# Kernel optimization log

Hardware: AMD Instinct MI355X
Metric: run time of the kernel (lower is better)

## Reference

```python
import jax, jax.numpy as jnp
import numpy as np

N_NODES = 50000
K_CHEB = 3


def _norm_weights(edge_index, num_nodes):
    # PyG ChebConv with normalization='sym', lambda_max=2.0:
    # L_hat = (2/lambda_max) * (I - D^-1/2 A D^-1/2) - I = -D^-1/2 A D^-1/2
    src, dst = edge_index[0], edge_index[1]
    ones = jnp.ones(src.shape[0], dtype=jnp.float32)
    deg = jax.ops.segment_sum(ones, src, num_segments=num_nodes)
    dis = jnp.where(deg > 0, jax.lax.rsqrt(jnp.maximum(deg, 1.0)), 0.0)
    w = dis[src] * dis[dst]  # [E]
    return src, dst, w


def _cheb_conv(x, src, dst, w, W, b, num_nodes):
    # W: [K, in, out], b: [out]
    def lap(v):  # L_hat @ v = -(D^-1/2 A D^-1/2) v via gather + segment-sum
        return -jax.ops.segment_sum(w[:, None] * v[src], dst, num_segments=num_nodes)
    Tx0 = x
    out = Tx0 @ W[0]
    Tx1 = lap(x)
    out = out + Tx1 @ W[1]
    for k in range(2, W.shape[0]):
        Tx2 = 2.0 * lap(Tx1) - Tx0
        out = out + Tx2 @ W[k]
        Tx0, Tx1 = Tx1, Tx2
    return out + b


def setup_inputs() -> dict:
    key = jax.random.key(0)
    ks = jax.random.split(key, 9)
    N, E, F_IN, F_HID, F_OUT = N_NODES, 800000, 128, 64, 16
    x = jax.random.normal(ks[0], (N, F_IN), dtype=jnp.float32)
    edge_index = jax.random.randint(ks[1], (2, E), 0, N, dtype=jnp.int64)
    def glorot(k, kk, fi, fo):
        s = (6.0 / (fi + fo)) ** 0.5
        return jax.random.uniform(k, (kk, fi, fo), jnp.float32, -s, s)
    W1 = glorot(ks[2], K_CHEB, F_IN, F_HID)
    b1 = jnp.zeros((F_HID,), jnp.float32)
    Wm = glorot(ks[3], K_CHEB, F_HID, F_HID)
    bm = jnp.zeros((F_HID,), jnp.float32)
    W2 = glorot(ks[4], K_CHEB, F_HID, F_OUT)
    b2 = jnp.zeros((F_OUT,), jnp.float32)
    return {"x": x, "edge_index": edge_index, "W1": W1, "b1": b1,
            "Wm": Wm, "bm": bm, "W2": W2, "b2": b2}


def reference(x, edge_index, W1, b1, Wm, bm, W2, b2):
    src, dst, w = _norm_weights(edge_index, N_NODES)
    h = jax.nn.relu(_cheb_conv(x, src, dst, w, W1, b1, N_NODES))
    # dropout is identity in eval mode (training=False)
    h = jax.nn.relu(_cheb_conv(h, src, dst, w, Wm, bm, N_NODES))
    out = _cheb_conv(h, src, dst, w, W2, b2, N_NODES)
    return out
```

## Files before the change

### kernel.cpp

```cpp
#include <hip/hip_runtime.h>
#include <hip/hip_fp16.h>

constexpr int NNODES = 50000;
constexpr int NS  = 64;
constexpr int NR  = 4;
constexpr int RSZ = 12500;

typedef _Float16 half8_t __attribute__((ext_vector_type(8)));
typedef _Float16 half4_t __attribute__((ext_vector_type(4)));
typedef float    f32x4_t __attribute__((ext_vector_type(4)));

template<int CH> struct hvec_sel;
template<> struct hvec_sel<4> { using T = half4_t; };
template<> struct hvec_sel<8> { using T = half8_t; };


__global__ void __launch_bounds__(256) hist_kernel(const int* __restrict__ ei, int E, int ES,
                                                   int* __restrict__ part_src,
                                                   int* __restrict__ part_dst) {
  __shared__ int sh[RSZ];
  for (int i = threadIdx.x; i < RSZ; i += 256) sh[i] = 0;
  __syncthreads();
  const int s = blockIdx.x, r = blockIdx.y, z = blockIdx.z;
  const int lo = r * RSZ;
  const int* __restrict__ idxarr = ei + (z ? E : 0);
  const int e0 = s * ES, e1 = min(e0 + ES, E);
  for (int e = e0 + (int)threadIdx.x; e < e1; e += 256) {
    unsigned u = (unsigned)(idxarr[e] - lo);
    if (u < (unsigned)RSZ) atomicAdd(&sh[u], 1);
  }
  __syncthreads();
  int* __restrict__ part = z ? part_dst : part_src;
  const int base = (s * NR + r) * RSZ;
  for (int i = threadIdx.x; i < RSZ; i += 256) part[base + i] = sh[i];
}

__global__ void __launch_bounds__(256) reduce_kernel(const int* __restrict__ part_src,
                                                     int* __restrict__ part_dst,
                                                     float* __restrict__ dis,
                                                     int* __restrict__ cnt_dst, int N) {
  int n = blockIdx.x * 256 + threadIdx.x;
  if (n >= N) return;
  int r = n / RSZ, i = n - r * RSZ;
  int ssum = 0;
  #pragma unroll 4
  for (int s = 0; s < NS; ++s) ssum += part_src[(size_t)(s * NR + r) * RSZ + i];
  dis[n] = (ssum > 0) ? rsqrtf((float)ssum) : 0.0f;
  int off = 0;
  for (int s = 0; s < NS; ++s) {
    size_t idx = (size_t)(s * NR + r) * RSZ + i;
    int c = part_dst[idx];
    part_dst[idx] = off;
    off += c;
  }
  cnt_dst[n] = off;
}

__global__ void __launch_bounds__(256) scan1_kernel(const int* __restrict__ cnt,
                                                    int* __restrict__ exc,
                                                    int* __restrict__ bsum, int N) {
  __shared__ int sh[256];
  int tid = threadIdx.x;
  int i = blockIdx.x * 256 + tid;
  int v = (i < N) ? cnt[i] : 0;
  int acc = v;
  sh[tid] = acc; __syncthreads();
  #pragma unroll
  for (int off = 1; off < 256; off <<= 1) {
    int t = (tid >= off) ? sh[tid - off] : 0;
    __syncthreads();
    acc += t;
    sh[tid] = acc;
    __syncthreads();
  }
  if (i < N) exc[i] = acc - v;
  if (tid == 255) bsum[blockIdx.x] = acc;
}

__global__ void __launch_bounds__(256) scan2_kernel(int* __restrict__ bsum, int NB) {
  __shared__ int sh[256];
  int tid = threadIdx.x;
  int v = (tid < NB) ? bsum[tid] : 0;
  int acc = v;
  sh[tid] = acc; __syncthreads();
  #pragma unroll
  for (int off = 1; off < 256; off <<= 1) {
    int t = (tid >= off) ? sh[tid - off] : 0;
    __syncthreads();
    acc += t;
    sh[tid] = acc;
    __syncthreads();
  }
  if (tid < NB) bsum[tid] = acc - v;
}

__global__ void __launch_bounds__(256) scan3_kernel(int* __restrict__ exc,
                                                    const int* __restrict__ bsum, int N) {
  int i = blockIdx.x * 256 + threadIdx.x;
  if (i < N) exc[i] += bsum[blockIdx.x];
}

__global__ void __launch_bounds__(256) fill_kernel(const int* __restrict__ ei, int E, int ES,
                                                   const int* __restrict__ startv,
                                                   const int* __restrict__ pd_off,
                                                   const float* __restrict__ dis,
                                                   int2* __restrict__ ew) {
  __shared__ int cur[RSZ];
  for (int i = threadIdx.x; i < RSZ; i += 256) cur[i] = 0;
  __syncthreads();
  const int s = blockIdx.x, r = blockIdx.y;
  const int lo = r * RSZ;
  const int base = (s * NR + r) * RSZ;
  const int e0 = s * ES, e1 = min(e0 + ES, E);
  for (int e = e0 + (int)threadIdx.x; e < e1; e += 256) {
    int sv = ei[e], d = ei[E + e];
    unsigned u = (unsigned)(d - lo);
    if (u < (unsigned)RSZ) {
      int rank = atomicAdd(&cur[u], 1);
      int pos = startv[d] + pd_off[base + u] + rank;
      float w = -dis[sv] * dis[d];
      ew[pos] = make_int2(sv, __float_as_int(w));
    }
  }
}

template<int FIN, int FOUT>
__global__ void __launch_bounds__(256) pack_kernel(const float* __restrict__ W,
                                                   _Float16* __restrict__ Bp) {
  constexpr int NT = 3 * FOUT / 16;
  constexpr int KT = FIN / 32;
  const int total = KT * NT * 512;
  for (int i = blockIdx.x * 256 + threadIdx.x; i < total; i += gridDim.x * 256) {
    int j = i & 7;
    int lane = (i >> 3) & 63;
    int tile = i >> 9;
    int nt = tile % NT, kt = tile / NT;
    int k = kt * 32 + (lane >> 4) * 8 + j;
    int n = nt * 16 + (lane & 15);
    int cheb = n / FOUT, c = n - cheb * FOUT;
    Bp[i] = (_Float16)W[((size_t)cheb * FIN + k) * FOUT + c];
  }
}

template<int FIN, int FOUT, typename IN_T>
__global__ void __launch_bounds__(256) gemm_mfma_kernel(const IN_T* __restrict__ X,
    const _Float16* __restrict__ Bp, const float* __restrict__ b,
    _Float16* __restrict__ A, _Float16* __restrict__ U, _Float16* __restrict__ V, int N) {
  constexpr int NT = 3 * FOUT / 16;
  constexpr int C3 = NT / 3;
  constexpr int KT = FIN / 32;
  constexpr int LDR = FIN + 8;
  __shared__ _Float16 xs[64 * LDR];

  const int tid = threadIdx.x;
  const int row0 = blockIdx.x * 64;

  for (int i = tid * 4; i < 64 * FIN; i += 1024) {
    int r = i / FIN, k = i - r * FIN;
    int row = row0 + r;
    short4 hv = make_short4(0, 0, 0, 0);
    if (row < N) {
      if constexpr (sizeof(IN_T) == 4) {
        float4 v = *(const float4*)((const float*)X + (size_t)row * FIN + k);
        _Float16 h0 = (_Float16)v.x, h1 = (_Float16)v.y, h2 = (_Float16)v.z, h3 = (_Float16)v.w;
        hv = make_short4(*(short*)&h0, *(short*)&h1, *(short*)&h2, *(short*)&h3);
      } else {
        hv = *(const short4*)((const _Float16*)X + (size_t)row * FIN + k);
      }
    }
    *(short4*)(&xs[r * LDR + k]) = hv;
  }
  __syncthreads();

  const int wave = tid >> 6, lane = tid & 63;
  const int m = lane & 15, quad = lane >> 4;

  f32x4_t acc[NT];
  #pragma unroll
  for (int nt = 0; nt < NT; ++nt) acc[nt] = (f32x4_t){0.f, 0.f, 0.f, 0.f};

  #pragma unroll
  for (int kt = 0; kt < KT; ++kt) {
    half8_t a = *(const half8_t*)(&xs[(wave * 16 + m) * LDR + kt * 32 + quad * 8]);
    const half8_t* bp = (const half8_t*)Bp + (size_t)(kt * NT) * 64 + lane;
    #pragma unroll
    for (int nt = 0; nt < NT; ++nt) {
      half8_t bf = bp[(size_t)nt * 64];
      acc[nt] = __builtin_amdgcn_mfma_f32_16x16x32_f16(a, bf, acc[nt], 0, 0, 0);
    }
  }

  const int row_b = row0 + wave * 16 + quad * 4;
  #pragma unroll
  for (int nt = 0; nt < C3; ++nt) {
    int c = nt * 16 + m;
    float bb = b[c];
    #pragma unroll
    for (int r = 0; r < 4; ++r) {
      int row = row_b + r;
      if (row < N) {
        size_t o = (size_t)row * FOUT + c;
        A[o] = (_Float16)(acc[nt][r] - acc[nt + 2 * C3][r] + bb);
        U[o] = (_Float16)acc[nt + C3][r];
        V[o] = (_Float16)acc[nt + 2 * C3][r];
      }
    }
  }
}


template<int F, int CH>
__global__ void __launch_bounds__(256) lapA_kernel(const void* __restrict__ Vp,
    const void* __restrict__ Up, void* __restrict__ Yp,
    const int* __restrict__ start, const int* __restrict__ cnt,
    const int2* __restrict__ ew, int N) {
  using HT = typename hvec_sel<CH>::T;
  constexpr int H = F / CH;
  const HT* __restrict__ Vv = (const HT*)Vp;
  int t = blockIdx.x * 256 + threadIdx.x;
  int n = t / H;
  if (n >= N) return;
  int h = t - n * H;
  int j = start[n], e = j + cnt[n];
  float acc[CH];
  #pragma unroll
  for (int i = 0; i < CH; ++i) acc[i] = 0.f;
  for (; j + 3 < e; j += 4) {
    int2 cc0 = ew[j], cc1 = ew[j + 1], cc2 = ew[j + 2], cc3 = ew[j + 3];
    HT v0 = Vv[(size_t)cc0.x * H + h];
    HT v1 = Vv[(size_t)cc1.x * H + h];
    HT v2 = Vv[(size_t)cc2.x * H + h];
    HT v3 = Vv[(size_t)cc3.x * H + h];
    float w0 = __int_as_float(cc0.y), w1 = __int_as_float(cc1.y);
    float w2 = __int_as_float(cc2.y), w3 = __int_as_float(cc3.y);
    #pragma unroll
    for (int i = 0; i < CH; ++i) {
      acc[i] = fmaf(w0, (float)v0[i], acc[i]);
      acc[i] = fmaf(w1, (float)v1[i], acc[i]);
      acc[i] = fmaf(w2, (float)v2[i], acc[i]);
      acc[i] = fmaf(w3, (float)v3[i], acc[i]);
    }
  }
  for (; j < e; ++j) {
    int2 c = ew[j];
    float w = __int_as_float(c.y);
    HT v = Vv[(size_t)c.x * H + h];
    #pragma unroll
    for (int i = 0; i < CH; ++i) acc[i] = fmaf(w, (float)v[i], acc[i]);
  }
  HT u = ((const HT*)Up)[t];
  HT y;
  #pragma unroll
  for (int i = 0; i < CH; ++i) y[i] = (_Float16)fmaf(2.f, acc[i], (float)u[i]);
  ((HT*)Yp)[t] = y;
}

template<int F, int CH, bool RELU, bool OUT32>
__global__ void __launch_bounds__(256) lapB_kernel(const void* __restrict__ Yp,
    const void* __restrict__ Ap,
    const int* __restrict__ start, const int* __restrict__ cnt,
    const int2* __restrict__ ew, void* __restrict__ outp, int N) {
  using HT = typename hvec_sel<CH>::T;
  constexpr int H = F / CH;
  const HT* __restrict__ Yv = (const HT*)Yp;
  int t = blockIdx.x * 256 + threadIdx.x;
  int n = t / H;
  if (n >= N) return;
  int h = t - n * H;
  int j = start[n], e = j + cnt[n];
  float acc[CH];
  #pragma unroll
  for (int i = 0; i < CH; ++i) acc[i] = 0.f;
  for (; j + 3 < e; j += 4) {
    int2 cc0 = ew[j], cc1 = ew[j + 1], cc2 = ew[j + 2], cc3 = ew[j + 3];
    HT v0 = Yv[(size_t)cc0.x * H + h];
    HT v1 = Yv[(size_t)cc1.x * H + h];
    HT v2 = Yv[(size_t)cc2.x * H + h];
    HT v3 = Yv[(size_t)cc3.x * H + h];
    float w0 = __int_as_float(cc0.y), w1 = __int_as_float(cc1.y);
    float w2 = __int_as_float(cc2.y), w3 = __int_as_float(cc3.y);
    #pragma unroll
    for (int i = 0; i < CH; ++i) {
      acc[i] = fmaf(w0, (float)v0[i], acc[i]);
      acc[i] = fmaf(w1, (float)v1[i], acc[i]);
      acc[i] = fmaf(w2, (float)v2[i], acc[i]);
      acc[i] = fmaf(w3, (float)v3[i], acc[i]);
    }
  }
  for (; j < e; ++j) {
    int2 c = ew[j];
    float w = __int_as_float(c.y);
    HT v = Yv[(size_t)c.x * H + h];
    #pragma unroll
    for (int i = 0; i < CH; ++i) acc[i] = fmaf(w, (float)v[i], acc[i]);
  }
  HT a = ((const HT*)Ap)[t];
  float r[CH];
  #pragma unroll
  for (int i = 0; i < CH; ++i) {
    r[i] = (float)a[i] + acc[i];
    if (RELU) r[i] = fmaxf(r[i], 0.f);
  }
  if constexpr (OUT32) {
    float4* o4 = (float4*)outp;
    #pragma unroll
    for (int q = 0; q < CH / 4; ++q)
      o4[(size_t)t * (CH / 4) + q] = make_float4(r[4 * q], r[4 * q + 1], r[4 * q + 2], r[4 * q + 3]);
  } else {
    HT y;
    #pragma unroll
    for (int i = 0; i < CH; ++i) y[i] = (_Float16)r[i];
    ((HT*)outp)[t] = y;
  }
}


extern "C" void kernel_launch(void* const* d_in, const int* in_sizes, int n_in,
                              void* d_out, int out_size, void* d_ws, size_t ws_size,
                              hipStream_t stream) {
  const float* x  = (const float*)d_in[0];
  const int*   ei = (const int*)d_in[1];
  const float* W1 = (const float*)d_in[2];
  const float* b1 = (const float*)d_in[3];
  const float* Wm = (const float*)d_in[4];
  const float* bm = (const float*)d_in[5];
  const float* W2 = (const float*)d_in[6];
  const float* b2 = (const float*)d_in[7];
  float* out = (float*)d_out;
  const int N = NNODES;
  const int E = in_sizes[1] / 2;
  const int ES = (E + NS - 1) / NS;
  const int NB = (N + 255) / 256;

  char* p = (char*)d_ws;
  auto alloc = [&](size_t bytes) -> char* {
    char* q = p;
    p += (bytes + 255) & ~(size_t)255;
    return q;
  };
  int*      part_src = (int*)alloc((size_t)NS * NR * RSZ * 4);
  int*      part_dst = (int*)alloc((size_t)NS * NR * RSZ * 4);
  int*      cnt_dst  = (int*)alloc((size_t)N * 4);
  int*      startv   = (int*)alloc((size_t)N * 4);
  int*      bsum     = (int*)alloc(1024);
  float*    dis      = (float*)alloc((size_t)N * 4);
  int2*     ew       = (int2*)alloc((size_t)E * 8);
  _Float16* Xh       = (_Float16*)alloc((size_t)N * 64 * 2);
  _Float16* Ah       = (_Float16*)alloc((size_t)N * 64 * 2);
  _Float16* Uh       = (_Float16*)alloc((size_t)N * 64 * 2);
  _Float16* Vh       = (_Float16*)alloc((size_t)N * 64 * 2);
  _Float16* Yh       = (_Float16*)alloc((size_t)N * 64 * 2);
  _Float16* Bp1      = (_Float16*)alloc((size_t)128 * 192 * 2);
  _Float16* Bp2      = (_Float16*)alloc((size_t)64 * 192 * 2);
  _Float16* Bp3      = (_Float16*)alloc((size_t)64 * 48 * 2);

  hist_kernel<<<dim3(NS, NR, 2), 256, 0, stream>>>(ei, E, ES, part_src, part_dst);
  reduce_kernel<<<NB, 256, 0, stream>>>(part_src, part_dst, dis, cnt_dst, N);
  scan1_kernel<<<NB, 256, 0, stream>>>(cnt_dst, startv, bsum, N);
  scan2_kernel<<<1, 256, 0, stream>>>(bsum, NB);
  scan3_kernel<<<NB, 256, 0, stream>>>(startv, bsum, N);
  fill_kernel<<<dim3(NS, NR), 256, 0, stream>>>(ei, E, ES, startv, part_dst, dis, ew);

  pack_kernel<128, 64><<<24, 256, 0, stream>>>(W1, Bp1);
  pack_kernel<64, 64><<<12, 256, 0, stream>>>(Wm, Bp2);
  pack_kernel<64, 16><<<3, 256, 0, stream>>>(W2, Bp3);

  const int gmm  = (N + 63) / 64;
  const int g64c = (N * 8 + 255) / 256;
  const int g16c = (N * 4 + 255) / 256;

  gemm_mfma_kernel<128, 64, float><<<gmm, 256, 0, stream>>>(x, Bp1, b1, Ah, Uh, Vh, N);
  lapA_kernel<64, 8><<<g64c, 256, 0, stream>>>(Vh, Uh, Yh, startv, cnt_dst, ew, N);
  lapB_kernel<64, 8, true, false><<<g64c, 256, 0, stream>>>(Yh, Ah, startv, cnt_dst, ew, Xh, N);

  gemm_mfma_kernel<64, 64, _Float16><<<gmm, 256, 0, stream>>>(Xh, Bp2, bm, Ah, Uh, Vh, N);
  lapA_kernel<64, 8><<<g64c, 256, 0, stream>>>(Vh, Uh, Yh, startv, cnt_dst, ew, N);
  lapB_kernel<64, 8, true, false><<<g64c, 256, 0, stream>>>(Yh, Ah, startv, cnt_dst, ew, Xh, N);

  gemm_mfma_kernel<64, 16, _Float16><<<gmm, 256, 0, stream>>>(Xh, Bp3, b2, Ah, Uh, Vh, N);
  lapA_kernel<16, 4><<<g16c, 256, 0, stream>>>(Vh, Uh, Yh, startv, cnt_dst, ew, N);
  lapB_kernel<16, 4, false, true><<<g16c, 256, 0, stream>>>(Yh, Ah, startv, cnt_dst, ew, out, N);
}
```

Before: 288.4 us.

## Merge preprocessing launches and overlap CSR fill with first GEMM; unroll gathers by 8

Merges the histogram and weight-packing kernels into one launch. Folds the reduce and first-level scan together and drops the scan3 pass by adding the block offset on the fly wherever a row start is read. The CSR fill blocks share one launch with the first-layer GEMM blocks so the two independent phases can run concurrently. The Laplacian gather loops are also unrolled to 8 edges per step to keep more loads in flight. The costs are an extra indirection per row-start lookup, a shared-memory footprint sized for the larger of the fill and GEMM users, and higher register pressure in the gather kernels.

```diff
diff --git a/kernel.cpp b/kernel.cpp
--- a/kernel.cpp
+++ b/kernel.cpp
@@ -15,122 +15,13 @@
 template<> struct hvec_sel<8> { using T = half8_t; };
 
 
-__global__ void __launch_bounds__(256) hist_kernel(const int* __restrict__ ei, int E, int ES,
-                                                   int* __restrict__ part_src,
-                                                   int* __restrict__ part_dst) {
-  __shared__ int sh[RSZ];
-  for (int i = threadIdx.x; i < RSZ; i += 256) sh[i] = 0;
-  __syncthreads();
-  const int s = blockIdx.x, r = blockIdx.y, z = blockIdx.z;
-  const int lo = r * RSZ;
-  const int* __restrict__ idxarr = ei + (z ? E : 0);
-  const int e0 = s * ES, e1 = min(e0 + ES, E);
-  for (int e = e0 + (int)threadIdx.x; e < e1; e += 256) {
-    unsigned u = (unsigned)(idxarr[e] - lo);
-    if (u < (unsigned)RSZ) atomicAdd(&sh[u], 1);
-  }
-  __syncthreads();
-  int* __restrict__ part = z ? part_dst : part_src;
-  const int base = (s * NR + r) * RSZ;
-  for (int i = threadIdx.x; i < RSZ; i += 256) part[base + i] = sh[i];
-}
-
-__global__ void __launch_bounds__(256) reduce_kernel(const int* __restrict__ part_src,
-                                                     int* __restrict__ part_dst,
-                                                     float* __restrict__ dis,
-                                                     int* __restrict__ cnt_dst, int N) {
-  int n = blockIdx.x * 256 + threadIdx.x;
-  if (n >= N) return;
-  int r = n / RSZ, i = n - r * RSZ;
-  int ssum = 0;
-  #pragma unroll 4
-  for (int s = 0; s < NS; ++s) ssum += part_src[(size_t)(s * NR + r) * RSZ + i];
-  dis[n] = (ssum > 0) ? rsqrtf((float)ssum) : 0.0f;
-  int off = 0;
-  for (int s = 0; s < NS; ++s) {
-    size_t idx = (size_t)(s * NR + r) * RSZ + i;
-    int c = part_dst[idx];
-    part_dst[idx] = off;
-    off += c;
-  }
-  cnt_dst[n] = off;
-}
-
-__global__ void __launch_bounds__(256) scan1_kernel(const int* __restrict__ cnt,
-                                                    int* __restrict__ exc,
-                                                    int* __restrict__ bsum, int N) {
-  __shared__ int sh[256];
-  int tid = threadIdx.x;
-  int i = blockIdx.x * 256 + tid;
-  int v = (i < N) ? cnt[i] : 0;
-  int acc = v;
-  sh[tid] = acc; __syncthreads();
-  #pragma unroll
-  for (int off = 1; off < 256; off <<= 1) {
-    int t = (tid >= off) ? sh[tid - off] : 0;
-    __syncthreads();
-    acc += t;
-    sh[tid] = acc;
-    __syncthreads();
-  }
-  if (i < N) exc[i] = acc - v;
-  if (tid == 255) bsum[blockIdx.x] = acc;
-}
-
-__global__ void __launch_bounds__(256) scan2_kernel(int* __restrict__ bsum, int NB) {
-  __shared__ int sh[256];
-  int tid = threadIdx.x;
-  int v = (tid < NB) ? bsum[tid] : 0;
-  int acc = v;
-  sh[tid] = acc; __syncthreads();
-  #pragma unroll
-  for (int off = 1; off < 256; off <<= 1) {
-    int t = (tid >= off) ? sh[tid - off] : 0;
-    __syncthreads();
-    acc += t;
-    sh[tid] = acc;
-    __syncthreads();
-  }
-  if (tid < NB) bsum[tid] = acc - v;
-}
-
-__global__ void __launch_bounds__(256) scan3_kernel(int* __restrict__ exc,
-                                                    const int* __restrict__ bsum, int N) {
-  int i = blockIdx.x * 256 + threadIdx.x;
-  if (i < N) exc[i] += bsum[blockIdx.x];
-}
-
-__global__ void __launch_bounds__(256) fill_kernel(const int* __restrict__ ei, int E, int ES,
-                                                   const int* __restrict__ startv,
-                                                   const int* __restrict__ pd_off,
-                                                   const float* __restrict__ dis,
-                                                   int2* __restrict__ ew) {
-  __shared__ int cur[RSZ];
-  for (int i = threadIdx.x; i < RSZ; i += 256) cur[i] = 0;
-  __syncthreads();
-  const int s = blockIdx.x, r = blockIdx.y;
-  const int lo = r * RSZ;
-  const int base = (s * NR + r) * RSZ;
-  const int e0 = s * ES, e1 = min(e0 + ES, E);
-  for (int e = e0 + (int)threadIdx.x; e < e1; e += 256) {
-    int sv = ei[e], d = ei[E + e];
-    unsigned u = (unsigned)(d - lo);
-    if (u < (unsigned)RSZ) {
-      int rank = atomicAdd(&cur[u], 1);
-      int pos = startv[d] + pd_off[base + u] + rank;
-      float w = -dis[sv] * dis[d];
-      ew[pos] = make_int2(sv, __float_as_int(w));
-    }
-  }
-}
-
 template<int FIN, int FOUT>
-__global__ void __launch_bounds__(256) pack_kernel(const float* __restrict__ W,
-                                                   _Float16* __restrict__ Bp) {
+__device__ void pack_dev(const float* __restrict__ W, _Float16* __restrict__ Bp,
+                         int b, int nb) {
   constexpr int NT = 3 * FOUT / 16;
   constexpr int KT = FIN / 32;
   const int total = KT * NT * 512;
-  for (int i = blockIdx.x * 256 + threadIdx.x; i < total; i += gridDim.x * 256) {
+  for (int i = b * 256 + (int)threadIdx.x; i < total; i += nb * 256) {
     int j = i & 7;
     int lane = (i >> 3) & 63;
     int tile = i >> 9;
@@ -143,17 +34,17 @@
 }
 
 template<int FIN, int FOUT, typename IN_T>
-__global__ void __launch_bounds__(256) gemm_mfma_kernel(const IN_T* __restrict__ X,
-    const _Float16* __restrict__ Bp, const float* __restrict__ b,
-    _Float16* __restrict__ A, _Float16* __restrict__ U, _Float16* __restrict__ V, int N) {
+__device__ void gemm_dev(const IN_T* __restrict__ X, const _Float16* __restrict__ Bp,
+                         const float* __restrict__ b, _Float16* __restrict__ A,
+                         _Float16* __restrict__ U, _Float16* __restrict__ V,
+                         int N, int blk, _Float16* xs) {
   constexpr int NT = 3 * FOUT / 16;
   constexpr int C3 = NT / 3;
   constexpr int KT = FIN / 32;
   constexpr int LDR = FIN + 8;
-  __shared__ _Float16 xs[64 * LDR];
 
   const int tid = threadIdx.x;
-  const int row0 = blockIdx.x * 64;
+  const int row0 = blk * 64;
 
   for (int i = tid * 4; i < 64 * FIN; i += 1024) {
     int r = i / FIN, k = i - r * FIN;
@@ -209,10 +100,135 @@
 }
 
 
+__global__ void __launch_bounds__(256) k1_hist_pack(const int* __restrict__ ei, int E, int ES,
+    int* __restrict__ part_src, int* __restrict__ part_dst,
+    const float* __restrict__ W1, const float* __restrict__ Wm, const float* __restrict__ W2,
+    _Float16* __restrict__ Bp1, _Float16* __restrict__ Bp2, _Float16* __restrict__ Bp3) {
+  __shared__ int sh[RSZ];
+  const int bid = blockIdx.x;
+  if (bid < 512) {
+    const int z = bid & 1, r = (bid >> 1) & 3, s = bid >> 3;
+    for (int i = threadIdx.x; i < RSZ; i += 256) sh[i] = 0;
+    __syncthreads();
+    const int lo = r * RSZ;
+    const int* __restrict__ idxarr = ei + (z ? E : 0);
+    const int e0 = s * ES, e1 = min(e0 + ES, E);
+    for (int e = e0 + (int)threadIdx.x; e < e1; e += 256) {
+      unsigned u = (unsigned)(idxarr[e] - lo);
+      if (u < (unsigned)RSZ) atomicAdd(&sh[u], 1);
+    }
+    __syncthreads();
+    int* __restrict__ part = z ? part_dst : part_src;
+    const int base = (s * NR + r) * RSZ;
+    for (int i = threadIdx.x; i < RSZ; i += 256) part[base + i] = sh[i];
+  } else if (bid < 536) {
+    pack_dev<128, 64>(W1, Bp1, bid - 512, 24);
+  } else if (bid < 548) {
+    pack_dev<64, 64>(Wm, Bp2, bid - 536, 12);
+  } else {
+    pack_dev<64, 16>(W2, Bp3, bid - 548, 3);
+  }
+}
+
+
+__global__ void __launch_bounds__(256) k2_reduce_scan(const int* __restrict__ part_src,
+    int* __restrict__ part_dst, float* __restrict__ dis, int* __restrict__ cnt,
+    int* __restrict__ exc, int* __restrict__ bsum, int N) {
+  __shared__ int sh[256];
+  const int tid = threadIdx.x;
+  const int n = blockIdx.x * 256 + tid;
+  int off = 0;
+  if (n < N) {
+    int r = n / RSZ, i = n - r * RSZ;
+    int ssum = 0;
+    #pragma unroll 4
+    for (int s = 0; s < NS; ++s) ssum += part_src[(size_t)(s * NR + r) * RSZ + i];
+    dis[n] = (ssum > 0) ? rsqrtf((float)ssum) : 0.0f;
+    for (int s = 0; s < NS; ++s) {
+      size_t idx = (size_t)(s * NR + r) * RSZ + i;
+      int c = part_dst[idx];
+      part_dst[idx] = off;
+      off += c;
+    }
+    cnt[n] = off;
+  }
+  int acc = off;
+  sh[tid] = acc; __syncthreads();
+  #pragma unroll
+  for (int o = 1; o < 256; o <<= 1) {
+    int t = (tid >= o) ? sh[tid - o] : 0;
+    __syncthreads();
+    acc += t;
+    sh[tid] = acc;
+    __syncthreads();
+  }
+  if (n < N) exc[n] = acc - off;
+  if (tid == 255) bsum[blockIdx.x] = acc;
+}
+
+
+__global__ void __launch_bounds__(256) k2b_scan2(int* __restrict__ bsum, int NB) {
+  __shared__ int sh[256];
+  int tid = threadIdx.x;
+  int v = (tid < NB) ? bsum[tid] : 0;
+  int acc = v;
+  sh[tid] = acc; __syncthreads();
+  #pragma unroll
+  for (int o = 1; o < 256; o <<= 1) {
+    int t = (tid >= o) ? sh[tid - o] : 0;
+    __syncthreads();
+    acc += t;
+    sh[tid] = acc;
+    __syncthreads();
+  }
+  if (tid < NB) bsum[tid] = acc - v;
+}
+
+
+__global__ void __launch_bounds__(256) k3_fill_gemm1(const int* __restrict__ ei, int E, int ES,
+    const int* __restrict__ exc, const int* __restrict__ bsumx,
+    const int* __restrict__ pd_off, const float* __restrict__ dis, int2* __restrict__ ew,
+    const float* __restrict__ x, const _Float16* __restrict__ Bp1, const float* __restrict__ b1,
+    _Float16* __restrict__ Ah, _Float16* __restrict__ Uh, _Float16* __restrict__ Vh, int N) {
+  __shared__ __align__(16) char smem[50048];
+  const int bid = blockIdx.x;
+  if (bid < 256) {
+    int* cur = (int*)smem;
+    for (int i = threadIdx.x; i < RSZ; i += 256) cur[i] = 0;
+    __syncthreads();
+    const int s = bid >> 2, r = bid & 3;
+    const int lo = r * RSZ;
+    const int base = (s * NR + r) * RSZ;
+    const int e0 = s * ES, e1 = min(e0 + ES, E);
+    for (int e = e0 + (int)threadIdx.x; e < e1; e += 256) {
+      int sv = ei[e], d = ei[E + e];
+      unsigned u = (unsigned)(d - lo);
+      if (u < (unsigned)RSZ) {
+        int rank = atomicAdd(&cur[u], 1);
+        int pos = exc[d] + bsumx[d >> 8] + pd_off[base + u] + rank;
+        float w = -dis[sv] * dis[d];
+        ew[pos] = make_int2(sv, __float_as_int(w));
+      }
+    }
+  } else {
+    gemm_dev<128, 64, float>(x, Bp1, b1, Ah, Uh, Vh, N, bid - 256, (_Float16*)smem);
+  }
+}
+
+
+template<int FIN, int FOUT>
+__global__ void __launch_bounds__(256) gemm_mfma_kernel(const _Float16* __restrict__ X,
+    const _Float16* __restrict__ Bp, const float* __restrict__ b,
+    _Float16* __restrict__ A, _Float16* __restrict__ U, _Float16* __restrict__ V, int N) {
+  __shared__ _Float16 xs[64 * (FIN + 8)];
+  gemm_dev<FIN, FOUT, _Float16>(X, Bp, b, A, U, V, N, blockIdx.x, xs);
+}
+
+
 template<int F, int CH>
 __global__ void __launch_bounds__(256) lapA_kernel(const void* __restrict__ Vp,
     const void* __restrict__ Up, void* __restrict__ Yp,
-    const int* __restrict__ start, const int* __restrict__ cnt,
+    const int* __restrict__ exc, const int* __restrict__ cnt, const int* __restrict__ bsumx,
     const int2* __restrict__ ew, int N) {
   using HT = typename hvec_sel<CH>::T;
   constexpr int H = F / CH;
@@ -221,24 +237,35 @@
   int n = t / H;
   if (n >= N) return;
   int h = t - n * H;
-  int j = start[n], e = j + cnt[n];
+  int j = exc[n] + bsumx[n >> 8];
+  int e = j + cnt[n];
   float acc[CH];
   #pragma unroll
   for (int i = 0; i < CH; ++i) acc[i] = 0.f;
+  for (; j + 7 < e; j += 8) {
+    int2 c[8]; HT v[8];
+    #pragma unroll
+    for (int q = 0; q < 8; ++q) c[q] = ew[j + q];
+    #pragma unroll
+    for (int q = 0; q < 8; ++q) v[q] = Vv[(size_t)c[q].x * H + h];
+    #pragma unroll
+    for (int q = 0; q < 8; ++q) {
+      float w = __int_as_float(c[q].y);
+      #pragma unroll
+      for (int i = 0; i < CH; ++i) acc[i] = fmaf(w, (float)v[q][i], acc[i]);
+    }
+  }
   for (; j + 3 < e; j += 4) {
-    int2 cc0 = ew[j], cc1 = ew[j + 1], cc2 = ew[j + 2], cc3 = ew[j + 3];
-    HT v0 = Vv[(size_t)cc0.x * H + h];
-    HT v1 = Vv[(size_t)cc1.x * H + h];
-    HT v2 = Vv[(size_t)cc2.x * H + h];
-    HT v3 = Vv[(size_t)cc3.x * H + h];
-    float w0 = __int_as_float(cc0.y), w1 = __int_as_float(cc1.y);
-    float w2 = __int_as_float(cc2.y), w3 = __int_as_float(cc3.y);
-    #pragma unroll
-    for (int i = 0; i < CH; ++i) {
-      acc[i] = fmaf(w0, (float)v0[i], acc[i]);
-      acc[i] = fmaf(w1, (float)v1[i], acc[i]);
-      acc[i] = fmaf(w2, (float)v2[i], acc[i]);
-      acc[i] = fmaf(w3, (float)v3[i], acc[i]);
+    int2 c[4]; HT v[4];
+    #pragma unroll
+    for (int q = 0; q < 4; ++q) c[q] = ew[j + q];
+    #pragma unroll
+    for (int q = 0; q < 4; ++q) v[q] = Vv[(size_t)c[q].x * H + h];
+    #pragma unroll
+    for (int q = 0; q < 4; ++q) {
+      float w = __int_as_float(c[q].y);
+      #pragma unroll
+      for (int i = 0; i < CH; ++i) acc[i] = fmaf(w, (float)v[q][i], acc[i]);
     }
   }
   for (; j < e; ++j) {
@@ -258,7 +285,7 @@
 template<int F, int CH, bool RELU, bool OUT32>
 __global__ void __launch_bounds__(256) lapB_kernel(const void* __restrict__ Yp,
     const void* __restrict__ Ap,
-    const int* __restrict__ start, const int* __restrict__ cnt,
+    const int* __restrict__ exc, const int* __restrict__ cnt, const int* __restrict__ bsumx,
     const int2* __restrict__ ew, void* __restrict__ outp, int N) {
   using HT = typename hvec_sel<CH>::T;
   constexpr int H = F / CH;
@@ -267,24 +294,35 @@
   int n = t / H;
   if (n >= N) return;
   int h = t - n * H;
-  int j = start[n], e = j + cnt[n];
+  int j = exc[n] + bsumx[n >> 8];
+  int e = j + cnt[n];
   float acc[CH];
   #pragma unroll
   for (int i = 0; i < CH; ++i) acc[i] = 0.f;
+  for (; j + 7 < e; j += 8) {
+    int2 c[8]; HT v[8];
+    #pragma unroll
+    for (int q = 0; q < 8; ++q) c[q] = ew[j + q];
+    #pragma unroll
+    for (int q = 0; q < 8; ++q) v[q] = Yv[(size_t)c[q].x * H + h];
+    #pragma unroll
+    for (int q = 0; q < 8; ++q) {
+      float w = __int_as_float(c[q].y);
+      #pragma unroll
+      for (int i = 0; i < CH; ++i) acc[i] = fmaf(w, (float)v[q][i], acc[i]);
+    }
+  }
   for (; j + 3 < e; j += 4) {
-    int2 cc0 = ew[j], cc1 = ew[j + 1], cc2 = ew[j + 2], cc3 = ew[j + 3];
-    HT v0 = Yv[(size_t)cc0.x * H + h];
-    HT v1 = Yv[(size_t)cc1.x * H + h];
-    HT v2 = Yv[(size_t)cc2.x * H + h];
-    HT v3 = Yv[(size_t)cc3.x * H + h];
-    float w0 = __int_as_float(cc0.y), w1 = __int_as_float(cc1.y);
-    float w2 = __int_as_float(cc2.y), w3 = __int_as_float(cc3.y);
-    #pragma unroll
-    for (int i = 0; i < CH; ++i) {
-      acc[i] = fmaf(w0, (float)v0[i], acc[i]);
-      acc[i] = fmaf(w1, (float)v1[i], acc[i]);
-      acc[i] = fmaf(w2, (float)v2[i], acc[i]);
-      acc[i] = fmaf(w3, (float)v3[i], acc[i]);
+    int2 c[4]; HT v[4];
+    #pragma unroll
+    for (int q = 0; q < 4; ++q) c[q] = ew[j + q];
+    #pragma unroll
+    for (int q = 0; q < 4; ++q) v[q] = Yv[(size_t)c[q].x * H + h];
+    #pragma unroll
+    for (int q = 0; q < 4; ++q) {
+      float w = __int_as_float(c[q].y);
+      #pragma unroll
+      for (int i = 0; i < CH; ++i) acc[i] = fmaf(w, (float)v[q][i], acc[i]);
     }
   }
   for (; j < e; ++j) {
@@ -340,8 +378,8 @@
   };
   int*      part_src = (int*)alloc((size_t)NS * NR * RSZ * 4);
   int*      part_dst = (int*)alloc((size_t)NS * NR * RSZ * 4);
-  int*      cnt_dst  = (int*)alloc((size_t)N * 4);
-  int*      startv   = (int*)alloc((size_t)N * 4);
+  int*      cnt      = (int*)alloc((size_t)N * 4);
+  int*      exc      = (int*)alloc((size_t)N * 4);
   int*      bsum     = (int*)alloc(1024);
   float*    dis      = (float*)alloc((size_t)N * 4);
   int2*     ew       = (int2*)alloc((size_t)E * 8);
@@ -354,30 +392,25 @@
   _Float16* Bp2      = (_Float16*)alloc((size_t)64 * 192 * 2);
   _Float16* Bp3      = (_Float16*)alloc((size_t)64 * 48 * 2);
 
-  hist_kernel<<<dim3(NS, NR, 2), 256, 0, stream>>>(ei, E, ES, part_src, part_dst);
-  reduce_kernel<<<NB, 256, 0, stream>>>(part_src, part_dst, dis, cnt_dst, N);
-  scan1_kernel<<<NB, 256, 0, stream>>>(cnt_dst, startv, bsum, N);
-  scan2_kernel<<<1, 256, 0, stream>>>(bsum, NB);
-  scan3_kernel<<<NB, 256, 0, stream>>>(startv, bsum, N);
-  fill_kernel<<<dim3(NS, NR), 256, 0, stream>>>(ei, E, ES, startv, part_dst, dis, ew);
-
-  pack_kernel<128, 64><<<24, 256, 0, stream>>>(W1, Bp1);
-  pack_kernel<64, 64><<<12, 256, 0, stream>>>(Wm, Bp2);
-  pack_kernel<64, 16><<<3, 256, 0, stream>>>(W2, Bp3);
+  k1_hist_pack<<<551, 256, 0, stream>>>(ei, E, ES, part_src, part_dst,
+                                        W1, Wm, W2, Bp1, Bp2, Bp3);
+  k2_reduce_scan<<<NB, 256, 0, stream>>>(part_src, part_dst, dis, cnt, exc, bsum, N);
+  k2b_scan2<<<1, 256, 0, stream>>>(bsum, NB);
+  k3_fill_gemm1<<<256 + 782, 256, 0, stream>>>(ei, E, ES, exc, bsum, part_dst, dis, ew,
+                                               x, Bp1, b1, Ah, Uh, Vh, N);
 
   const int gmm  = (N + 63) / 64;
   const int g64c = (N * 8 + 255) / 256;
   const int g16c = (N * 4 + 255) / 256;
 
-  gemm_mfma_kernel<128, 64, float><<<gmm, 256, 0, stream>>>(x, Bp1, b1, Ah, Uh, Vh, N);
-  lapA_kernel<64, 8><<<g64c, 256, 0, stream>>>(Vh, Uh, Yh, startv, cnt_dst, ew, N);
-  lapB_kernel<64, 8, true, false><<<g64c, 256, 0, stream>>>(Yh, Ah, startv, cnt_dst, ew, Xh, N);
-
-  gemm_mfma_kernel<64, 64, _Float16><<<gmm, 256, 0, stream>>>(Xh, Bp2, bm, Ah, Uh, Vh, N);
-  lapA_kernel<64, 8><<<g64c, 256, 0, stream>>>(Vh, Uh, Yh, startv, cnt_dst, ew, N);
-  lapB_kernel<64, 8, true, false><<<g64c, 256, 0, stream>>>(Yh, Ah, startv, cnt_dst, ew, Xh, N);
-
-  gemm_mfma_kernel<64, 16, _Float16><<<gmm, 256, 0, stream>>>(Xh, Bp3, b2, Ah, Uh, Vh, N);
-  lapA_kernel<16, 4><<<g16c, 256, 0, stream>>>(Vh, Uh, Yh, startv, cnt_dst, ew, N);
-  lapB_kernel<16, 4, false, true><<<g16c, 256, 0, stream>>>(Yh, Ah, startv, cnt_dst, ew, out, N);
-}
+  lapA_kernel<64, 8><<<g64c, 256, 0, stream>>>(Vh, Uh, Yh, exc, cnt, bsum, ew, N);
+  lapB_kernel<64, 8, true, false><<<g64c, 256, 0, stream>>>(Yh, Ah, exc, cnt, bsum, ew, Xh, N);
+
+  gemm_mfma_kernel<64, 64><<<gmm, 256, 0, stream>>>(Xh, Bp2, bm, Ah, Uh, Vh, N);
+  lapA_kernel<64, 8><<<g64c, 256, 0, stream>>>(Vh, Uh, Yh, exc, cnt, bsum, ew, N);
+  lapB_kernel<64, 8, true, false><<<g64c, 256, 0, stream>>>(Yh, Ah, exc, cnt, bsum, ew, Xh, N);
+
+  gemm_mfma_kernel<64, 16><<<gmm, 256, 0, stream>>>(Xh, Bp3, b2, Ah, Uh, Vh, N);
+  lapA_kernel<16, 4><<<g16c, 256, 0, stream>>>(Vh, Uh, Yh, exc, cnt, bsum, ew, N);
+  lapB_kernel<16, 4, false, true><<<g16c, 256, 0, stream>>>(Yh, Ah, exc, cnt, bsum, ew, out, N);
+}
```

Measured after the change: 269.4 us. -6.6%, faster.
